# Optimization experiments

Hardware: AMD Instinct MI355X
Metric: run time of the kernel (lower is better)

Reference implementation:

```python
import jax, jax.numpy as jnp
import numpy as np

K = 5
PAD = K // 2
EPS = 1e-12  # F.normalize eps


def setup_inputs() -> dict:
    key = jax.random.key(0)
    k1, k2, k3 = jax.random.split(key, 3)
    b, c, h, w = 8, 1024, 64, 64
    out_ch = 1024
    feature = jax.random.normal(k1, (b, c, h, w), dtype=jnp.float32)
    # Conv2d(1024 + K*K, out_ch, 1) -> weight [out_ch, 1049], bias [out_ch]
    conv_w = jax.random.normal(k2, (out_ch, c + K * K), dtype=jnp.float32) * 0.02
    conv_b = jax.random.normal(k3, (out_ch,), dtype=jnp.float32) * 0.02
    return {"feature": feature, "conv_w": conv_w, "conv_b": conv_b}


def reference(feature, conv_w, conv_b):
    b, c, h, w = feature.shape
    # L2-normalize over channel dim (F.normalize: x / max(||x||, eps))
    norm = jnp.sqrt(jnp.sum(feature * feature, axis=1, keepdims=True))
    fn = feature / jnp.maximum(norm, EPS)
    fp = jnp.pad(fn, ((0, 0), (0, 0), (PAD, PAD), (PAD, PAD)))
    # 25 shifted correlations; order matches torch loop: index = col*K + row
    corr = jnp.stack(
        [jnp.sum(fp[:, :, r:h + r, cc:w + cc] * fn, axis=1)
         for cc in range(K) for r in range(K)],
        axis=1,
    )  # [b, K*K, h, w]
    cat = jnp.concatenate([feature, corr], axis=1)  # [b, c+K*K, h, w]
    y = jnp.einsum('oc,bchw->bohw', conv_w, cat) + conv_b[None, :, None, None]
    return jax.nn.relu(y)
```

## Files before the change

kernel.cpp:

```cpp
#include <hip/hip_runtime.h>
#include <hip/hip_bf16.h>


typedef __attribute__((ext_vector_type(8))) short short8x;
typedef __attribute__((ext_vector_type(4))) float floatx4;

#define B_   8
#define C_   1024
#define HW_  4096
#define KPAD 1056

__device__ __forceinline__ unsigned short f2bf(float f) {
  unsigned int u = __float_as_uint(f);
  u += 0x7FFFu + ((u >> 16) & 1u);
  return (unsigned short)(u >> 16);
}
__device__ __forceinline__ float bf2f(unsigned short s) {
  return __uint_as_float(((unsigned int)s) << 16);
}

__device__ __forceinline__ void async16(const void* g, void* l) {
  __builtin_amdgcn_global_load_lds(
      (__attribute__((address_space(1))) void*)(void*)g,
      (__attribute__((address_space(3))) void*)l, 16, 0, 0);
}

__global__ __launch_bounds__(512) void scn_corr_part(
    const float* __restrict__ f, float* __restrict__ part) {
  const int tid = threadIdx.x;
  const int x = tid & 63;
  const int y = blockIdx.x * 8 + (tid >> 6);
  const int cs = blockIdx.y, b = blockIdx.z;

  const int xs0 = (x + 2 < 64) ? x + 2 : 63;
  const int xs1 = (x + 1 < 64) ? x + 1 : 63;
  const int xs3 = (x - 1 >= 0) ? x - 1 : 0;
  const int xs4 = (x - 2 >= 0) ? x - 2 : 0;

  const bool ym2 = (y >= 2), ym1 = (y >= 1), yp1 = (y <= 62), yp2 = (y <= 61);

  const float* rp0 = f + ((size_t)b * C_ + cs * 128) * HW_ + y * 64;

  float h[25];
#pragma unroll
  for (int j = 0; j < 25; ++j) h[j] = 0.f;

#pragma unroll 4
  for (int c = 0; c < 128; ++c) {
    const float* rp = rp0 + (size_t)c * HW_;
    const float ctr = rp[x];
    const float vm2 = ym2 ? rp[x - 128] : 0.f;
    const float vm1 = ym1 ? rp[x - 64] : 0.f;
    const float vp1 = yp1 ? rp[x + 64] : 0.f;
    const float vp2 = yp2 ? rp[x + 128] : 0.f;
    const float c0 = rp[xs0], c1 = rp[xs1], c3 = rp[xs3], c4 = rp[xs4];
    const float v[5] = {vm2, vm1, ctr, vp1, vp2};
    const float cc[5] = {c0, c1, ctr, c3, c4};
#pragma unroll
    for (int dxi = 0; dxi < 5; ++dxi)
#pragma unroll
      for (int dyi = 0; dyi < 5; ++dyi)
        h[dxi * 5 + dyi] = fmaf(v[dyi], cc[dxi], h[dxi * 5 + dyi]);
  }

  float* pb = part + (size_t)(cs * 25) * 32768 + b * HW_ + y * 64;
#pragma unroll
  for (int j = 0; j < 25; ++j) {
    const int dx = (j / 5) - 2;
    const int tgt = x - dx;
    const int wx = (tgt + 64) & 63;
    const float val = ((unsigned)tgt < 64u) ? h[j] : 0.f;
    pb[(size_t)j * 32768 + wx] = val;
  }
}

__global__ __launch_bounds__(256) void scn_transpose(
    const float* __restrict__ f, unsigned short* __restrict__ At) {
  __shared__ float lds[64][65];
  const int mt = blockIdx.x, kt = blockIdx.y, b = blockIdx.z;
  const int tid = threadIdx.x;
  const float* src = f + ((size_t)b * C_ + kt * 64) * HW_ + mt * 64;
  const int mi = tid & 63, kr = tid >> 6;
#pragma unroll
  for (int i = 0; i < 16; ++i)
    lds[kr + i * 4][mi] = src[(size_t)(kr + i * 4) * HW_ + mi];
  __syncthreads();
  unsigned short* dst = At + ((size_t)b * HW_ + mt * 64) * KPAD + kt * 64;
  const int c = tid & 7, mr = tid >> 3;
#pragma unroll
  for (int half = 0; half < 2; ++half) {
    const int mm = mr + half * 32;
    short8x v;
#pragma unroll
    for (int j = 0; j < 8; ++j) v[j] = (short)f2bf(lds[c * 8 + j][mm]);
    *(short8x*)(dst + (size_t)mm * KPAD + c * 8) = v;
  }
}

__global__ __launch_bounds__(256) void scn_invn(const float* __restrict__ part,
                                                float* __restrict__ invn) {
  const int i = blockIdx.x * 256 + threadIdx.x;
  float s = 0.f;
#pragma unroll
  for (int cs = 0; cs < 8; ++cs) s += part[(size_t)(cs * 25 + 12) * 32768 + i];
  invn[i] = 1.0f / fmaxf(sqrtf(s), 1e-12f);
}

__global__ __launch_bounds__(256) void scn_corr_reduce(
    const float* __restrict__ part, const float* __restrict__ invn,
    unsigned short* __restrict__ At) {
  const int b = blockIdx.y;
  const int m = blockIdx.x * 256 + threadIdx.x;
  const int i = b * HW_ + m;
  const int y = m >> 6, x = m & 63;

  float acc[25];
#pragma unroll
  for (int j = 0; j < 25; ++j) acc[j] = 0.f;
#pragma unroll 1
  for (int cs = 0; cs < 8; ++cs) {
    const float* pb = part + (size_t)(cs * 25) * 32768 + i;
#pragma unroll
    for (int j = 0; j < 25; ++j) acc[j] += pb[(size_t)j * 32768];
  }
  const float ic = invn[i];
  unsigned short r[32];
#pragma unroll
  for (int j = 0; j < 25; ++j) {
    const int dy = (j % 5) - 2, dx = (j / 5) - 2;
    const int ny = y + dy, nx = x + dx;
    float in2 = (ny >= 0 && ny < 64 && nx >= 0 && nx < 64)
                    ? invn[b * HW_ + (ny << 6) + nx] : 0.f;
    r[j] = f2bf(acc[j] * ic * in2);
  }
#pragma unroll
  for (int j = 25; j < 32; ++j) r[j] = 0;
  unsigned short* row = At + ((size_t)b * HW_ + m) * KPAD + 1024;
#pragma unroll
  for (int v = 0; v < 4; ++v) *(short8x*)(row + v * 8) = *(short8x*)(r + v * 8);
}

__global__ __launch_bounds__(256) void scn_wcast(const float* __restrict__ w,
                                                 unsigned short* __restrict__ Wb) {
  const int i = blockIdx.x * 256 + threadIdx.x;
  const int o = i / KPAD, k = i - o * KPAD;
  Wb[i] = (k < 1049) ? f2bf(w[(size_t)o * 1049 + k]) : 0;
}

__global__ __launch_bounds__(256) void scn_gemm(
    const unsigned short* __restrict__ Wb, const unsigned short* __restrict__ At,
    const float* __restrict__ bias, float* __restrict__ out) {
  __shared__ __align__(16) unsigned short lA[128 * 32];
  __shared__ __align__(16) unsigned short lB[128 * 32];
  const int tid = threadIdx.x;
  const int nb = blockIdx.x, ob = blockIdx.y, b = blockIdx.z;

  const int srow = tid >> 2;
  const int skc = (tid & 3) * 8;
  const unsigned short* gW0 = Wb + (size_t)(ob * 128 + srow) * KPAD + skc;
  const unsigned short* gW1 = gW0 + (size_t)64 * KPAD;
  const unsigned short* gB0 = At + ((size_t)b * HW_ + nb * 128 + srow) * KPAD + skc;
  const unsigned short* gB1 = gB0 + (size_t)64 * KPAD;
  char* dA0 = (char*)lA + tid * 16;
  char* dA1 = (char*)lA + 4096 + tid * 16;
  char* dB0 = (char*)lB + tid * 16;
  char* dB1 = (char*)lB + 4096 + tid * 16;

  const int w = tid >> 6, l = tid & 63;
  const int wm = (w & 1) << 6, wn = (w >> 1) << 6;
  const int l16 = l & 15, l4 = l >> 4;
  const unsigned short* rA = lA + (wm + l16) * 32 + l4 * 8;
  const unsigned short* rB = lB + (wn + l16) * 32 + l4 * 8;

  floatx4 acc[4][4];
#pragma unroll
  for (int i = 0; i < 4; ++i)
#pragma unroll
    for (int j = 0; j < 4; ++j) acc[i][j] = (floatx4){0.f, 0.f, 0.f, 0.f};

  for (int kt = 0; kt < 33; ++kt) {
    const int ko = kt * 32;
    async16(gW0 + ko, dA0);
    async16(gW1 + ko, dA1);
    async16(gB0 + ko, dB0);
    async16(gB1 + ko, dB1);
    __syncthreads();
    short8x a[4], bb[4];
#pragma unroll
    for (int i = 0; i < 4; ++i) a[i] = *(const short8x*)(rA + i * 16 * 32);
#pragma unroll
    for (int j = 0; j < 4; ++j) bb[j] = *(const short8x*)(rB + j * 16 * 32);
#pragma unroll
    for (int i = 0; i < 4; ++i)
#pragma unroll
      for (int j = 0; j < 4; ++j)
        acc[i][j] =
            __builtin_amdgcn_mfma_f32_16x16x32_bf16(a[i], bb[j], acc[i][j], 0, 0, 0);
    __syncthreads();
  }

  float* outb = out + (size_t)b * C_ * HW_;
#pragma unroll
  for (int i = 0; i < 4; ++i) {
    const int o0 = ob * 128 + wm + i * 16 + l4 * 4;
    float bs[4];
#pragma unroll
    for (int r = 0; r < 4; ++r) bs[r] = bias[o0 + r];
#pragma unroll
    for (int j = 0; j < 4; ++j) {
      const int m = nb * 128 + wn + j * 16 + l16;
#pragma unroll
      for (int r = 0; r < 4; ++r) {
        float v = acc[i][j][r] + bs[r];
        outb[(size_t)(o0 + r) * HW_ + m] = v > 0.f ? v : 0.f;
      }
    }
  }
}

extern "C" void kernel_launch(void* const* d_in, const int* in_sizes, int n_in,
                              void* d_out, int out_size, void* d_ws, size_t ws_size,
                              hipStream_t stream) {
  const float* feature = (const float*)d_in[0];
  const float* conv_w  = (const float*)d_in[1];
  const float* conv_b  = (const float*)d_in[2];
  float* out = (float*)d_out;

  char* ws = (char*)d_ws;
  unsigned short* At = (unsigned short*)(ws);
  float* part        = (float*)(ws + 69206016);
  unsigned short* Wb = (unsigned short*)(ws + 95420416);
  float* invn        = (float*)(ws + 97583104);

  scn_corr_part<<<dim3(8, 8, 8), 512, 0, stream>>>(feature, part);
  scn_transpose<<<dim3(64, 16, 8), 256, 0, stream>>>(feature, At);
  scn_invn<<<dim3(128), 256, 0, stream>>>(part, invn);
  scn_corr_reduce<<<dim3(16, 8), 256, 0, stream>>>(part, invn, At);
  scn_wcast<<<dim3((1024 * KPAD) / 256), 256, 0, stream>>>(conv_w, Wb);
  scn_gemm<<<dim3(32, 8, 8), 256, 0, stream>>>(Wb, At, conv_b, out);
}
```

Baseline: 442.9 us.

## Rewrite GEMM with 256x256 tiles, double-buffered swizzled LDS and phased MFMA schedule

The bf16 GEMM moves from 128x128 tiles with K=32 steps to 256x256 tiles with K=64 steps, run by 512-thread blocks. Loads go through a double-buffered async global-to-LDS path with an XOR swizzle, and the MFMA work is split into four phases with barriers, s_setprio and prefetch of the tile two steps ahead. K is padded to 1088 so it divides into 64-wide steps, and the workspace layout is rearranged. The aim is more operand reuse and overlap of memory with MFMA. The cost is 128KB of dynamic LDS, high register pressure from 128 accumulator floats per thread, and Wb now sharing its workspace offset with part.

```diff
diff --git a/kernel.cpp b/kernel.cpp
--- a/kernel.cpp
+++ b/kernel.cpp
@@ -8,7 +8,8 @@
 #define B_   8
 #define C_   1024
 #define HW_  4096
-#define KPAD 1056
+#define KPAD 1088
+#define NT   17
 
 __device__ __forceinline__ unsigned short f2bf(float f) {
   unsigned int u = __float_as_uint(f);
@@ -23,6 +24,10 @@
   __builtin_amdgcn_global_load_lds(
       (__attribute__((address_space(1))) void*)(void*)g,
       (__attribute__((address_space(3))) void*)l, 16, 0, 0);
+}
+
+__device__ __forceinline__ short8x rd16(const char* p) {
+  return *(const short8x*)p;
 }
 
 __global__ __launch_bounds__(512) void scn_corr_part(
@@ -124,7 +129,7 @@
     for (int j = 0; j < 25; ++j) acc[j] += pb[(size_t)j * 32768];
   }
   const float ic = invn[i];
-  unsigned short r[32];
+  unsigned short r[64];
 #pragma unroll
   for (int j = 0; j < 25; ++j) {
     const int dy = (j % 5) - 2, dx = (j / 5) - 2;
@@ -134,10 +139,10 @@
     r[j] = f2bf(acc[j] * ic * in2);
   }
 #pragma unroll
-  for (int j = 25; j < 32; ++j) r[j] = 0;
+  for (int j = 25; j < 64; ++j) r[j] = 0;
   unsigned short* row = At + ((size_t)b * HW_ + m) * KPAD + 1024;
 #pragma unroll
-  for (int v = 0; v < 4; ++v) *(short8x*)(row + v * 8) = *(short8x*)(r + v * 8);
+  for (int v = 0; v < 8; ++v) *(short8x*)(row + v * 8) = *(short8x*)(r + v * 8);
 }
 
 __global__ __launch_bounds__(256) void scn_wcast(const float* __restrict__ w,
@@ -147,68 +152,159 @@
   Wb[i] = (k < 1049) ? f2bf(w[(size_t)o * 1049 + k]) : 0;
 }
 
-__global__ __launch_bounds__(256) void scn_gemm(
+__global__ __launch_bounds__(512, 2) void scn_gemm(
     const unsigned short* __restrict__ Wb, const unsigned short* __restrict__ At,
     const float* __restrict__ bias, float* __restrict__ out) {
-  __shared__ __align__(16) unsigned short lA[128 * 32];
-  __shared__ __align__(16) unsigned short lB[128 * 32];
+  extern __shared__ char lds[];
   const int tid = threadIdx.x;
+  const int l = tid & 63;
+  const int wid = tid >> 6;
+  const int wm = wid >> 2;
+  const int wn = wid & 3;
   const int nb = blockIdx.x, ob = blockIdx.y, b = blockIdx.z;
 
-  const int srow = tid >> 2;
-  const int skc = (tid & 3) * 8;
-  const unsigned short* gW0 = Wb + (size_t)(ob * 128 + srow) * KPAD + skc;
-  const unsigned short* gW1 = gW0 + (size_t)64 * KPAD;
-  const unsigned short* gB0 = At + ((size_t)b * HW_ + nb * 128 + srow) * KPAD + skc;
-  const unsigned short* gB1 = gB0 + (size_t)64 * KPAD;
-  char* dA0 = (char*)lA + tid * 16;
-  char* dA1 = (char*)lA + 4096 + tid * 16;
-  char* dB0 = (char*)lB + tid * 16;
-  char* dB1 = (char*)lB + 4096 + tid * 16;
-
-  const int w = tid >> 6, l = tid & 63;
-  const int wm = (w & 1) << 6, wn = (w >> 1) << 6;
-  const int l16 = l & 15, l4 = l >> 4;
-  const unsigned short* rA = lA + (wm + l16) * 32 + l4 * 8;
-  const unsigned short* rB = lB + (wn + l16) * 32 + l4 * 8;
-
-  floatx4 acc[4][4];
-#pragma unroll
-  for (int i = 0; i < 4; ++i)
+  const int rr = tid >> 3;
+  const int cswz = ((tid & 7) ^ (rr & 7)) << 3;
+  const unsigned short* gA = Wb + (size_t)(ob * 256 + rr) * KPAD + cswz;
+  const unsigned short* gB = At + ((size_t)b * HW_ + nb * 256 + rr) * KPAD + cswz;
+  char* const dBase = (char*)lds + tid * 16;
+
+#define ISSUE_A(bf, kt)                                         \
+  do {                                                          \
+    const unsigned short* _s = gA + (kt) * 64;                  \
+    char* _d = dBase + (bf) * 65536;                            \
+    async16(_s, _d);                                            \
+    async16(_s + (size_t)64 * KPAD, _d + 8192);                 \
+    async16(_s + (size_t)128 * KPAD, _d + 16384);               \
+    async16(_s + (size_t)192 * KPAD, _d + 24576);               \
+  } while (0)
+
+#define ISSUE_B(bf, kt)                                         \
+  do {                                                          \
+    const unsigned short* _s = gB + (kt) * 64;                  \
+    char* _d = dBase + (bf) * 65536 + 32768;                    \
+    async16(_s, _d);                                            \
+    async16(_s + (size_t)64 * KPAD, _d + 8192);                 \
+    async16(_s + (size_t)128 * KPAD, _d + 16384);               \
+    async16(_s + (size_t)192 * KPAD, _d + 24576);               \
+  } while (0)
+
+  const int l15 = l & 15, l4g = l >> 4, l7 = l & 7;
+  const int aoff0 = l15 * 128 + ((l4g ^ l7) << 4);
+  const int aoff1 = l15 * 128 + (((l4g + 4) ^ l7) << 4);
+  const char* aB0 = (const char*)lds + wm * 16384;
+  const char* bB0 = (const char*)lds + 32768 + (wn >> 1) * 16384 + (wn & 1) * 8192;
+
+  floatx4 acc[8][4];
+#pragma unroll
+  for (int i = 0; i < 8; ++i)
 #pragma unroll
     for (int j = 0; j < 4; ++j) acc[i][j] = (floatx4){0.f, 0.f, 0.f, 0.f};
 
-  for (int kt = 0; kt < 33; ++kt) {
-    const int ko = kt * 32;
-    async16(gW0 + ko, dA0);
-    async16(gW1 + ko, dA1);
-    async16(gB0 + ko, dB0);
-    async16(gB1 + ko, dB1);
-    __syncthreads();
-    short8x a[4], bb[4];
-#pragma unroll
-    for (int i = 0; i < 4; ++i) a[i] = *(const short8x*)(rA + i * 16 * 32);
-#pragma unroll
-    for (int j = 0; j < 4; ++j) bb[j] = *(const short8x*)(rB + j * 16 * 32);
+  ISSUE_A(0, 0); ISSUE_B(0, 0);
+  ISSUE_A(1, 1); ISSUE_B(1, 1);
+  asm volatile("s_waitcnt vmcnt(8)" ::: "memory");
+  __builtin_amdgcn_s_barrier();
+
+  short8x a[4][2], b0[2][2], b1[2][2];
+
+  for (int t = 0; t < NT; ++t) {
+    const int bf = t & 1;
+    const char* ab = aB0 + bf * 65536;
+    const char* bb = bB0 + bf * 65536;
+    const int t2 = (t < NT - 2) ? (t + 2) : 0;
+
+#pragma unroll
+    for (int i = 0; i < 4; ++i) {
+      a[i][0] = rd16(ab + i * 2048 + aoff0);
+      a[i][1] = rd16(ab + i * 2048 + aoff1);
+    }
+#pragma unroll
+    for (int j = 0; j < 2; ++j) {
+      b0[j][0] = rd16(bb + j * 2048 + aoff0);
+      b0[j][1] = rd16(bb + j * 2048 + aoff1);
+    }
+    __builtin_amdgcn_s_barrier();
+    asm volatile("s_waitcnt lgkmcnt(0)" ::: "memory");
+    __builtin_amdgcn_sched_barrier(0);
+    __builtin_amdgcn_s_setprio(1);
 #pragma unroll
     for (int i = 0; i < 4; ++i)
 #pragma unroll
-      for (int j = 0; j < 4; ++j)
-        acc[i][j] =
-            __builtin_amdgcn_mfma_f32_16x16x32_bf16(a[i], bb[j], acc[i][j], 0, 0, 0);
-    __syncthreads();
-  }
+      for (int j = 0; j < 2; ++j) {
+        acc[i][j] = __builtin_amdgcn_mfma_f32_16x16x32_bf16(a[i][0], b0[j][0], acc[i][j], 0, 0, 0);
+        acc[i][j] = __builtin_amdgcn_mfma_f32_16x16x32_bf16(a[i][1], b0[j][1], acc[i][j], 0, 0, 0);
+      }
+    __builtin_amdgcn_s_setprio(0);
+    __builtin_amdgcn_s_barrier();
+
+#pragma unroll
+    for (int j = 0; j < 2; ++j) {
+      b1[j][0] = rd16(bb + (2 + j) * 2048 + aoff0);
+      b1[j][1] = rd16(bb + (2 + j) * 2048 + aoff1);
+    }
+    __builtin_amdgcn_s_barrier();
+    asm volatile("s_waitcnt lgkmcnt(0)" ::: "memory");
+    __builtin_amdgcn_sched_barrier(0);
+    __builtin_amdgcn_s_setprio(1);
+#pragma unroll
+    for (int i = 0; i < 4; ++i)
+#pragma unroll
+      for (int j = 0; j < 2; ++j) {
+        acc[i][2 + j] = __builtin_amdgcn_mfma_f32_16x16x32_bf16(a[i][0], b1[j][0], acc[i][2 + j], 0, 0, 0);
+        acc[i][2 + j] = __builtin_amdgcn_mfma_f32_16x16x32_bf16(a[i][1], b1[j][1], acc[i][2 + j], 0, 0, 0);
+      }
+    __builtin_amdgcn_s_setprio(0);
+    __builtin_amdgcn_s_barrier();
+
+#pragma unroll
+    for (int i = 0; i < 4; ++i) {
+      a[i][0] = rd16(ab + (4 + i) * 2048 + aoff0);
+      a[i][1] = rd16(ab + (4 + i) * 2048 + aoff1);
+    }
+    ISSUE_B(bf, t2);
+    __builtin_amdgcn_s_barrier();
+    asm volatile("s_waitcnt lgkmcnt(0)" ::: "memory");
+    __builtin_amdgcn_sched_barrier(0);
+    __builtin_amdgcn_s_setprio(1);
+#pragma unroll
+    for (int i = 0; i < 4; ++i)
+#pragma unroll
+      for (int j = 0; j < 2; ++j) {
+        acc[4 + i][2 + j] = __builtin_amdgcn_mfma_f32_16x16x32_bf16(a[i][0], b1[j][0], acc[4 + i][2 + j], 0, 0, 0);
+        acc[4 + i][2 + j] = __builtin_amdgcn_mfma_f32_16x16x32_bf16(a[i][1], b1[j][1], acc[4 + i][2 + j], 0, 0, 0);
+      }
+    __builtin_amdgcn_s_setprio(0);
+    __builtin_amdgcn_s_barrier();
+
+    ISSUE_A(bf, t2);
+    __builtin_amdgcn_s_barrier();
+    __builtin_amdgcn_s_setprio(1);
+#pragma unroll
+    for (int i = 0; i < 4; ++i)
+#pragma unroll
+      for (int j = 0; j < 2; ++j) {
+        acc[4 + i][j] = __builtin_amdgcn_mfma_f32_16x16x32_bf16(a[i][0], b0[j][0], acc[4 + i][j], 0, 0, 0);
+        acc[4 + i][j] = __builtin_amdgcn_mfma_f32_16x16x32_bf16(a[i][1], b0[j][1], acc[4 + i][j], 0, 0, 0);
+      }
+    __builtin_amdgcn_s_setprio(0);
+    asm volatile("s_waitcnt vmcnt(8)" ::: "memory");
+    __builtin_amdgcn_s_barrier();
+  }
+  asm volatile("s_waitcnt vmcnt(0)" ::: "memory");
+#undef ISSUE_A
+#undef ISSUE_B
 
   float* outb = out + (size_t)b * C_ * HW_;
 #pragma unroll
-  for (int i = 0; i < 4; ++i) {
-    const int o0 = ob * 128 + wm + i * 16 + l4 * 4;
+  for (int i = 0; i < 8; ++i) {
+    const int o0 = ob * 256 + wm * 128 + i * 16 + l4g * 4;
     float bs[4];
 #pragma unroll
     for (int r = 0; r < 4; ++r) bs[r] = bias[o0 + r];
 #pragma unroll
     for (int j = 0; j < 4; ++j) {
-      const int m = nb * 128 + wn + j * 16 + l16;
+      const int m = nb * 256 + wn * 64 + j * 16 + l15;
 #pragma unroll
       for (int r = 0; r < 4; ++r) {
         float v = acc[i][j][r] + bs[r];
@@ -228,14 +324,21 @@
 
   char* ws = (char*)d_ws;
   unsigned short* At = (unsigned short*)(ws);
-  float* part        = (float*)(ws + 69206016);
-  unsigned short* Wb = (unsigned short*)(ws + 95420416);
-  float* invn        = (float*)(ws + 97583104);
+  float* part        = (float*)(ws + 71303168);
+  unsigned short* Wb = (unsigned short*)(ws + 71303168);
+  float* invn        = (float*)(ws + 97517568);
+
+  static int gemm_attr_set = 0;
+  if (!gemm_attr_set) {
+    hipFuncSetAttribute((const void*)scn_gemm,
+                        hipFuncAttributeMaxDynamicSharedMemorySize, 131072);
+    gemm_attr_set = 1;
+  }
 
   scn_corr_part<<<dim3(8, 8, 8), 512, 0, stream>>>(feature, part);
   scn_transpose<<<dim3(64, 16, 8), 256, 0, stream>>>(feature, At);
   scn_invn<<<dim3(128), 256, 0, stream>>>(part, invn);
   scn_corr_reduce<<<dim3(16, 8), 256, 0, stream>>>(part, invn, At);
   scn_wcast<<<dim3((1024 * KPAD) / 256), 256, 0, stream>>>(conv_w, Wb);
-  scn_gemm<<<dim3(32, 8, 8), 256, 0, stream>>>(Wb, At, conv_b, out);
-}
+  scn_gemm<<<dim3(16, 4, 8), 512, 131072, stream>>>(Wb, At, conv_b, out);
+}
```

Result: faster. 383.2 us (-13.5%).

## Rewrite GEMM with 256x256 tiles, 4-stage async LDS pipeline and swizzle

Applied to the files above, without the earlier changes.

The GEMM moves from 128x128 tiles with 256 threads and a single LDS buffer to 512-thread blocks. Each block computes a 256x256 output tile per pass and makes two passes over adjacent column blocks. Operand tiles go through a four-deep ring of global_load_lds stages in 128 KB of dynamic LDS, with an XOR swizzle, partial vmcnt waits and setprio around the MFMA bursts, so loads overlap compute and operand reuse rises. The correlation partials use 4 channel splits instead of 8, the transpose uses float4 loads, K padding grows to 1088, and part and Wb share workspace. The large LDS footprint limits occupancy to one block per CU and leaves exactly 256 blocks, so there is little slack for load imbalance.

```diff
diff --git a/kernel.cpp b/kernel.cpp
--- a/kernel.cpp
+++ b/kernel.cpp
@@ -8,21 +8,25 @@
 #define B_   8
 #define C_   1024
 #define HW_  4096
-#define KPAD 1056
+#define KPAD 1088
+#define CS_  4
+#define CCH  256
+#define NKT  34
 
 __device__ __forceinline__ unsigned short f2bf(float f) {
   unsigned int u = __float_as_uint(f);
   u += 0x7FFFu + ((u >> 16) & 1u);
   return (unsigned short)(u >> 16);
 }
-__device__ __forceinline__ float bf2f(unsigned short s) {
-  return __uint_as_float(((unsigned int)s) << 16);
-}
 
 __device__ __forceinline__ void async16(const void* g, void* l) {
   __builtin_amdgcn_global_load_lds(
       (__attribute__((address_space(1))) void*)(void*)g,
       (__attribute__((address_space(3))) void*)l, 16, 0, 0);
+}
+
+__device__ __forceinline__ short8x rd16(const char* p) {
+  return *(const short8x*)p;
 }
 
 __global__ __launch_bounds__(512) void scn_corr_part(
@@ -39,14 +43,14 @@
 
   const bool ym2 = (y >= 2), ym1 = (y >= 1), yp1 = (y <= 62), yp2 = (y <= 61);
 
-  const float* rp0 = f + ((size_t)b * C_ + cs * 128) * HW_ + y * 64;
+  const float* rp0 = f + ((size_t)b * C_ + cs * CCH) * HW_ + y * 64;
 
   float h[25];
 #pragma unroll
   for (int j = 0; j < 25; ++j) h[j] = 0.f;
 
 #pragma unroll 4
-  for (int c = 0; c < 128; ++c) {
+  for (int c = 0; c < CCH; ++c) {
     const float* rp = rp0 + (size_t)c * HW_;
     const float ctr = rp[x];
     const float vm2 = ym2 ? rp[x - 128] : 0.f;
@@ -79,11 +83,14 @@
   __shared__ float lds[64][65];
   const int mt = blockIdx.x, kt = blockIdx.y, b = blockIdx.z;
   const int tid = threadIdx.x;
-  const float* src = f + ((size_t)b * C_ + kt * 64) * HW_ + mt * 64;
-  const int mi = tid & 63, kr = tid >> 6;
-#pragma unroll
-  for (int i = 0; i < 16; ++i)
-    lds[kr + i * 4][mi] = src[(size_t)(kr + i * 4) * HW_ + mi];
+  const int m4 = (tid & 15) << 2, kr0 = tid >> 4;
+  const float* src = f + ((size_t)b * C_ + kt * 64 + kr0) * HW_ + mt * 64 + m4;
+#pragma unroll
+  for (int i = 0; i < 4; ++i) {
+    floatx4 v = *(const floatx4*)(src + (size_t)i * 16 * HW_);
+    float* d = &lds[kr0 + i * 16][m4];
+    d[0] = v[0]; d[1] = v[1]; d[2] = v[2]; d[3] = v[3];
+  }
   __syncthreads();
   unsigned short* dst = At + ((size_t)b * HW_ + mt * 64) * KPAD + kt * 64;
   const int c = tid & 7, mr = tid >> 3;
@@ -102,7 +109,7 @@
   const int i = blockIdx.x * 256 + threadIdx.x;
   float s = 0.f;
 #pragma unroll
-  for (int cs = 0; cs < 8; ++cs) s += part[(size_t)(cs * 25 + 12) * 32768 + i];
+  for (int cs = 0; cs < CS_; ++cs) s += part[(size_t)(cs * 25 + 12) * 32768 + i];
   invn[i] = 1.0f / fmaxf(sqrtf(s), 1e-12f);
 }
 
@@ -118,13 +125,13 @@
 #pragma unroll
   for (int j = 0; j < 25; ++j) acc[j] = 0.f;
 #pragma unroll 1
-  for (int cs = 0; cs < 8; ++cs) {
+  for (int cs = 0; cs < CS_; ++cs) {
     const float* pb = part + (size_t)(cs * 25) * 32768 + i;
 #pragma unroll
     for (int j = 0; j < 25; ++j) acc[j] += pb[(size_t)j * 32768];
   }
   const float ic = invn[i];
-  unsigned short r[32];
+  unsigned short r[64];
 #pragma unroll
   for (int j = 0; j < 25; ++j) {
     const int dy = (j % 5) - 2, dx = (j / 5) - 2;
@@ -134,10 +141,10 @@
     r[j] = f2bf(acc[j] * ic * in2);
   }
 #pragma unroll
-  for (int j = 25; j < 32; ++j) r[j] = 0;
+  for (int j = 25; j < 64; ++j) r[j] = 0;
   unsigned short* row = At + ((size_t)b * HW_ + m) * KPAD + 1024;
 #pragma unroll
-  for (int v = 0; v < 4; ++v) *(short8x*)(row + v * 8) = *(short8x*)(r + v * 8);
+  for (int v = 0; v < 8; ++v) *(short8x*)(row + v * 8) = *(short8x*)(r + v * 8);
 }
 
 __global__ __launch_bounds__(256) void scn_wcast(const float* __restrict__ w,
@@ -147,75 +154,103 @@
   Wb[i] = (k < 1049) ? f2bf(w[(size_t)o * 1049 + k]) : 0;
 }
 
-__global__ __launch_bounds__(256) void scn_gemm(
+__global__ __launch_bounds__(512, 2) void scn_gemm(
     const unsigned short* __restrict__ Wb, const unsigned short* __restrict__ At,
     const float* __restrict__ bias, float* __restrict__ out) {
-  __shared__ __align__(16) unsigned short lA[128 * 32];
-  __shared__ __align__(16) unsigned short lB[128 * 32];
+  extern __shared__ char lds[];
   const int tid = threadIdx.x;
-  const int nb = blockIdx.x, ob = blockIdx.y, b = blockIdx.z;
-
-  const int srow = tid >> 2;
-  const int skc = (tid & 3) * 8;
-  const unsigned short* gW0 = Wb + (size_t)(ob * 128 + srow) * KPAD + skc;
-  const unsigned short* gW1 = gW0 + (size_t)64 * KPAD;
-  const unsigned short* gB0 = At + ((size_t)b * HW_ + nb * 128 + srow) * KPAD + skc;
-  const unsigned short* gB1 = gB0 + (size_t)64 * KPAD;
-  char* dA0 = (char*)lA + tid * 16;
-  char* dA1 = (char*)lA + 4096 + tid * 16;
-  char* dB0 = (char*)lB + tid * 16;
-  char* dB1 = (char*)lB + 4096 + tid * 16;
-
-  const int w = tid >> 6, l = tid & 63;
-  const int wm = (w & 1) << 6, wn = (w >> 1) << 6;
-  const int l16 = l & 15, l4 = l >> 4;
-  const unsigned short* rA = lA + (wm + l16) * 32 + l4 * 8;
-  const unsigned short* rB = lB + (wn + l16) * 32 + l4 * 8;
-
-  floatx4 acc[4][4];
-#pragma unroll
-  for (int i = 0; i < 4; ++i)
+  const int l = tid & 63;
+  const int wid = tid >> 6;
+  const int wm = wid >> 2, wn = wid & 3;
+  const int nb2 = blockIdx.x, ob = blockIdx.y, b = blockIdx.z;
+
+  const int r0 = tid >> 3, v0 = (tid & 7) ^ (r0 & 7);
+  const int r1 = (tid + 512) >> 3, v1 = (tid & 7) ^ (r1 & 7);
+  const unsigned short* gA0 =
+      Wb + (size_t)(ob * 256 + (v0 >> 2) * 128 + r0) * KPAD + (v0 & 3) * 8;
+  const unsigned short* gA1 =
+      Wb + (size_t)(ob * 256 + (v1 >> 2) * 128 + r1) * KPAD + (v1 & 3) * 8;
+  const unsigned short* gB0 =
+      At + ((size_t)b * HW_ + nb2 * 512 + (v0 >> 2) * 128 + r0) * KPAD + (v0 & 3) * 8;
+  const unsigned short* gB1 =
+      At + ((size_t)b * HW_ + nb2 * 512 + (v1 >> 2) * 128 + r1) * KPAD + (v1 & 3) * 8;
+
+#define STAGE(tau_) do {                                                \
+    int tau = (tau_); if (tau >= 2 * NKT) tau = 0;                      \
+    const int pass_ = (tau >= NKT) ? 1 : 0;                             \
+    const size_t ko = (size_t)(tau - NKT * pass_) * 32;                 \
+    const size_t bo = (size_t)pass_ * 256 * KPAD + ko;                  \
+    char* dst = lds + (size_t)(tau & 3) * 32768;                        \
+    async16(gA0 + ko, dst + tid * 16);                                  \
+    async16(gA1 + ko, dst + 8192 + tid * 16);                           \
+    async16(gB0 + bo, dst + 16384 + tid * 16);                          \
+    async16(gB1 + bo, dst + 24576 + tid * 16);                          \
+  } while (0)
+
+  const int l15 = l & 15, l4g = l >> 4, l7 = l & 7;
+  const int aoffc = l15 * 128 + (((wm * 4 + l4g) ^ l7) << 4);
+  const int boffc = ((wn & 1) * 64 + l15) * 128 +
+                    (((((wn >> 1) * 4) + l4g) ^ l7) << 4) + 16384;
+
+  floatx4 acc[8][4];
+#pragma unroll
+  for (int i = 0; i < 8; ++i)
 #pragma unroll
     for (int j = 0; j < 4; ++j) acc[i][j] = (floatx4){0.f, 0.f, 0.f, 0.f};
 
-  for (int kt = 0; kt < 33; ++kt) {
-    const int ko = kt * 32;
-    async16(gW0 + ko, dA0);
-    async16(gW1 + ko, dA1);
-    async16(gB0 + ko, dB0);
-    async16(gB1 + ko, dB1);
-    __syncthreads();
-    short8x a[4], bb[4];
-#pragma unroll
-    for (int i = 0; i < 4; ++i) a[i] = *(const short8x*)(rA + i * 16 * 32);
-#pragma unroll
-    for (int j = 0; j < 4; ++j) bb[j] = *(const short8x*)(rB + j * 16 * 32);
-#pragma unroll
-    for (int i = 0; i < 4; ++i)
-#pragma unroll
-      for (int j = 0; j < 4; ++j)
-        acc[i][j] =
-            __builtin_amdgcn_mfma_f32_16x16x32_bf16(a[i], bb[j], acc[i][j], 0, 0, 0);
-    __syncthreads();
-  }
-
-  float* outb = out + (size_t)b * C_ * HW_;
-#pragma unroll
-  for (int i = 0; i < 4; ++i) {
-    const int o0 = ob * 128 + wm + i * 16 + l4 * 4;
-    float bs[4];
-#pragma unroll
-    for (int r = 0; r < 4; ++r) bs[r] = bias[o0 + r];
-#pragma unroll
-    for (int j = 0; j < 4; ++j) {
-      const int m = nb * 128 + wn + j * 16 + l16;
-#pragma unroll
-      for (int r = 0; r < 4; ++r) {
-        float v = acc[i][j][r] + bs[r];
-        outb[(size_t)(o0 + r) * HW_ + m] = v > 0.f ? v : 0.f;
+  float* const outb = out + (size_t)b * C_ * HW_;
+  auto write_out = [&](int nbe) __attribute__((always_inline)) {
+#pragma unroll
+    for (int i = 0; i < 8; ++i) {
+      const int o0 = ob * 256 + wm * 128 + i * 16 + l4g * 4;
+      float bs[4];
+#pragma unroll
+      for (int r = 0; r < 4; ++r) bs[r] = bias[o0 + r];
+#pragma unroll
+      for (int j = 0; j < 4; ++j) {
+        const int m = nbe * 256 + wn * 64 + j * 16 + l15;
+#pragma unroll
+        for (int r = 0; r < 4; ++r) {
+          float v = acc[i][j][r] + bs[r];
+          outb[(size_t)(o0 + r) * HW_ + m] = v > 0.f ? v : 0.f;
+        }
       }
     }
-  }
+  };
+
+  STAGE(0); STAGE(1); STAGE(2);
+
+  for (int t = 0; t < 2 * NKT; ++t) {
+    const char* base = lds + (size_t)(t & 3) * 32768;
+    asm volatile("s_waitcnt vmcnt(8)" ::: "memory");
+    __builtin_amdgcn_s_barrier();
+    STAGE(t + 3);
+    short8x a[8], bfr[4];
+#pragma unroll
+    for (int i = 0; i < 8; ++i) a[i] = rd16(base + i * 2048 + aoffc);
+#pragma unroll
+    for (int j = 0; j < 4; ++j) bfr[j] = rd16(base + j * 2048 + boffc);
+    asm volatile("s_waitcnt lgkmcnt(0)" ::: "memory");
+    __builtin_amdgcn_sched_barrier(0);
+    __builtin_amdgcn_s_setprio(1);
+#pragma unroll
+    for (int i = 0; i < 8; ++i)
+#pragma unroll
+      for (int j = 0; j < 4; ++j)
+        acc[i][j] = __builtin_amdgcn_mfma_f32_16x16x32_bf16(a[i], bfr[j],
+                                                            acc[i][j], 0, 0, 0);
+    __builtin_amdgcn_s_setprio(0);
+    if (t == NKT - 1) {
+      write_out(nb2 * 2);
+#pragma unroll
+      for (int i = 0; i < 8; ++i)
+#pragma unroll
+        for (int j = 0; j < 4; ++j) acc[i][j] = (floatx4){0.f, 0.f, 0.f, 0.f};
+    }
+  }
+  asm volatile("s_waitcnt vmcnt(0)" ::: "memory");
+  write_out(nb2 * 2 + 1);
+#undef STAGE
 }
 
 extern "C" void kernel_launch(void* const* d_in, const int* in_sizes, int n_in,
@@ -228,14 +263,21 @@
 
   char* ws = (char*)d_ws;
   unsigned short* At = (unsigned short*)(ws);
-  float* part        = (float*)(ws + 69206016);
-  unsigned short* Wb = (unsigned short*)(ws + 95420416);
-  float* invn        = (float*)(ws + 97583104);
-
-  scn_corr_part<<<dim3(8, 8, 8), 512, 0, stream>>>(feature, part);
+  float* part        = (float*)(ws + 71303168);
+  unsigned short* Wb = (unsigned short*)(ws + 71303168);
+  float* invn        = (float*)(ws + 84410368);
+
+  static int gemm_attr_set = 0;
+  if (!gemm_attr_set) {
+    hipFuncSetAttribute((const void*)scn_gemm,
+                        hipFuncAttributeMaxDynamicSharedMemorySize, 131072);
+    gemm_attr_set = 1;
+  }
+
+  scn_corr_part<<<dim3(8, CS_, 8), 512, 0, stream>>>(feature, part);
   scn_transpose<<<dim3(64, 16, 8), 256, 0, stream>>>(feature, At);
   scn_invn<<<dim3(128), 256, 0, stream>>>(part, invn);
   scn_corr_reduce<<<dim3(16, 8), 256, 0, stream>>>(part, invn, At);
   scn_wcast<<<dim3((1024 * KPAD) / 256), 256, 0, stream>>>(conv_w, Wb);
-  scn_gemm<<<dim3(32, 8, 8), 256, 0, stream>>>(Wb, At, conv_b, out);
-}
+  scn_gemm<<<dim3(8, 4, 8), 512, 131072, stream>>>(Wb, At, conv_b, out);
+}
```

New measurement: 421.5 us. 4.8% less time.
